# Performance work log

Hardware: AMD Instinct MI355X
Metric: run time of the kernel (lower is better)

The kernel has to match this reference:

```python
import jax, jax.numpy as jnp
import numpy as np

B, T, C, H = 2, 2048, 1024, 16
N = C // H
TM_DIM, TD_DIM = 32, 64
EPS = 1e-5 * 8 ** 2  # GroupNorm eps from the module


def setup_inputs() -> dict:
    key = jax.random.key(0)
    ks = jax.random.split(key, 16)
    nrm = lambda k, shp, s: jax.random.normal(k, shp, dtype=jnp.float32) * s
    uni = lambda k, shp, a: jax.random.uniform(k, shp, jnp.float32, -a, a)
    ddd = (jnp.arange(C, dtype=jnp.float32) / C).reshape(1, 1, C)
    return {
        "x": nrm(ks[0], (B, T, C), 1.0),
        "time_maa_x": 1.0 - ddd ** 0.5,
        "time_maa_w": 1.0 - ddd ** 0.5,
        "time_maa_k": 1.0 - ddd ** 0.5,
        "time_maa_v": 1.0 - (ddd ** 0.5 + 0.15),
        "time_maa_r": 1.0 - ddd ** 0.25,
        "time_maa_g": 1.0 - ddd ** 0.25,
        "time_maa_w1": uni(ks[1], (C, 5 * TM_DIM), 1e-4),
        "time_maa_w2": uni(ks[2], (5, TM_DIM, C), 1e-4),
        "time_decay": jnp.linspace(-6.0, -1.0, C).astype(jnp.float32).reshape(1, 1, C),
        "time_decay_w1": uni(ks[3], (C, TD_DIM), 1e-4),
        "time_decay_w2": uni(ks[4], (TD_DIM, C), 1e-4),
        "time_faaaa": nrm(ks[5], (H, N), 0.1),
        "W_r": nrm(ks[6], (C, C), C ** -0.5),
        "W_k": nrm(ks[7], (C, C), C ** -0.5),
        "W_v": nrm(ks[8], (C, C), C ** -0.5),
        "W_g": nrm(ks[9], (C, C), C ** -0.5),
        "W_o": nrm(ks[10], (C, C), C ** -0.5),
        "ln_w": jnp.ones((C,), jnp.float32),
        "ln_b": jnp.zeros((C,), jnp.float32),
    }


def _forward(x, tmx, tmw, tmk, tmv, tmr, tmg, maa_w1, maa_w2, tdecay, td_w1,
             td_w2, u, Wr, Wk, Wv, Wg, Wo, ln_w, ln_b):
    Bq, Tq, Cq = x.shape
    # time_shift: x[t-1] with zero at t=0
    xx = jnp.concatenate([jnp.zeros_like(x[:, :1]), x[:, :-1]], axis=1) - x
    xxx = x + xx * tmx
    t5 = jnp.tanh(xxx @ maa_w1).reshape(Bq, Tq, 5, TM_DIM)
    m = jnp.einsum('btfe,fec->fbtc', t5, maa_w2)  # [5,B,T,C] data-dependent mix
    xw = x + xx * (tmw + m[0])
    xk = x + xx * (tmk + m[1])
    xv = x + xx * (tmv + m[2])
    xr = x + xx * (tmr + m[3])
    xg = x + xx * (tmg + m[4])
    r = xr @ Wr
    k = xk @ Wk
    v = xv @ Wv
    g = jax.nn.silu(xg @ Wg)
    w = tdecay + jnp.tanh(xw @ td_w1) @ td_w2          # [B,T,C] log-log decay
    decay = jnp.exp(-jnp.exp(w))                        # in (0,1)
    to_tbhn = lambda a: a.reshape(Bq, Tq, H, N).transpose(1, 0, 2, 3)
    rT, kT, vT, dT = (to_tbhn(a) for a in (r, k, v, decay))

    def step(S, inp):  # S: [B,H,N,N] (key_dim i, value_dim j)
        r_t, k_t, v_t, d_t = inp
        kv = k_t[..., :, None] * v_t[..., None, :]
        y = jnp.einsum('bhi,bhij->bhj', r_t, S + u[None, :, :, None] * kv)
        return d_t[..., None] * S + kv, y

    S0 = jnp.zeros((Bq, H, N, N), x.dtype)
    _, ys = jax.lax.scan(step, S0, (rT, kT, vT, dT))
    y = ys.transpose(1, 0, 2, 3).reshape(Bq, Tq, Cq)
    # GroupNorm with H groups over channels
    yh = y.reshape(Bq, Tq, H, N)
    mu = yh.mean(-1, keepdims=True)
    var = yh.var(-1, keepdims=True)
    yn = (yh - mu) / jnp.sqrt(var + EPS)
    yn = (yn * ln_w.reshape(H, N) + ln_b.reshape(H, N)).reshape(Bq, Tq, Cq)
    return (yn * g) @ Wo


def reference(x, time_maa_x, time_maa_w, time_maa_k, time_maa_v, time_maa_r,
              time_maa_g, time_maa_w1, time_maa_w2, time_decay, time_decay_w1,
              time_decay_w2, time_faaaa, W_r, W_k, W_v, W_g, W_o, ln_w, ln_b):
    return _forward(x, time_maa_x, time_maa_w, time_maa_k, time_maa_v,
                    time_maa_r, time_maa_g, time_maa_w1, time_maa_w2,
                    time_decay, time_decay_w1, time_decay_w2, time_faaaa,
                    W_r, W_k, W_v, W_g, W_o, ln_w, ln_b)
```

## Files before the change

### kernel.cpp

```cpp
#include <hip/hip_runtime.h>
#include <hip/hip_bf16.h>
#include <cstdint>
#include <cstddef>

#define B_ 2
#define T_ 2048
#define C_ 1024
#define H_ 16
#define NCH 32
#define CHL 64

typedef unsigned short ushort_t;
typedef __bf16 bf16x8 __attribute__((ext_vector_type(8)));
typedef float f32x4 __attribute__((ext_vector_type(4)));

__device__ __forceinline__ ushort_t f2bf(float f) {
  union { float f; uint32_t u; } x; x.f = f;
  uint32_t r = x.u + 0x7fffu + ((x.u >> 16) & 1u);
  return (ushort_t)(r >> 16);
}
__device__ __forceinline__ float bf2f(ushort_t h) {
  union { uint32_t u; float f; } x; x.u = (uint32_t)h << 16; return x.f;
}

__device__ __forceinline__ void gload16(const void* g, void* l) {
  __builtin_amdgcn_global_load_lds(
      (const __attribute__((address_space(1))) void*)g,
      (__attribute__((address_space(3))) void*)l, 16, 0, 0);
}

#define FENCE() asm volatile("" ::: "memory")
#define BAR() do { FENCE(); __builtin_amdgcn_s_barrier(); FENCE(); } while (0)

__device__ __forceinline__ void stb(ushort_t* tile, int row, int col, ushort_t v) {
  *(ushort_t*)((char*)tile + row * 128 + ((col * 2) ^ ((row & 7) << 4))) = v;
}
__device__ __forceinline__ bf16x8 ldb(const ushort_t* tile, int row, int kbyte) {
  return *(const bf16x8*)((const char*)tile + row * 128 + (kbyte ^ ((row & 7) << 4)));
}

struct TDesc { const float* src; ushort_t* dst; int R, Cc, Cpad; };
struct TArgs { TDesc d[9]; };

__global__ __launch_bounds__(256) void init_kernel(
    TArgs args, const float* __restrict__ x, const float* __restrict__ tmx,
    ushort_t* __restrict__ xh, ushort_t* __restrict__ xxh,
    ushort_t* __restrict__ xxx) {
  if (blockIdx.z < 9) {
    TDesc D = args.d[blockIdx.z];
    int c0 = blockIdx.x * 32, r0 = blockIdx.y * 32;
    if (c0 >= D.Cpad || r0 >= D.R) return;
    __shared__ float tile[32][33];
    int tx = threadIdx.x & 31, ty = threadIdx.x >> 5;
#pragma unroll
    for (int i = 0; i < 32; i += 8) {
      int r = r0 + ty + i, c = c0 + tx;
      tile[ty + i][tx] = (r < D.R && c < D.Cc) ? D.src[(size_t)r * D.Cc + c] : 0.f;
    }
    __syncthreads();
#pragma unroll
    for (int i = 0; i < 32; i += 8) {
      int c = c0 + ty + i, r = r0 + tx;
      if (c < D.Cpad && r < D.R) D.dst[(size_t)c * D.R + r] = f2bf(tile[tx][ty + i]);
    }
    return;
  }
  int lin = (blockIdx.y * 32 + blockIdx.x) * 256 + threadIdx.x;
#pragma unroll
  for (int rep = 0; rep < 4; ++rep) {
    size_t idx = ((size_t)(rep * 262144 + lin)) * 4;
    int tt = (int)((idx >> 10) & (T_ - 1));
    int c = (int)(idx & (C_ - 1));
    float4 xv = *(const float4*)&x[idx];
    float4 xp;
    if (tt == 0) { xp.x = xp.y = xp.z = xp.w = 0.f; }
    else xp = *(const float4*)&x[idx - C_];
    float4 tm = *(const float4*)&tmx[c];
    float4 d;
    d.x = xp.x - xv.x; d.y = xp.y - xv.y; d.z = xp.z - xv.z; d.w = xp.w - xv.w;
    ushort4 a, b, cc;
    a.x = f2bf(xv.x); a.y = f2bf(xv.y); a.z = f2bf(xv.z); a.w = f2bf(xv.w);
    b.x = f2bf(d.x);  b.y = f2bf(d.y);  b.z = f2bf(d.z);  b.w = f2bf(d.w);
    cc.x = f2bf(xv.x + d.x * tm.x); cc.y = f2bf(xv.y + d.y * tm.y);
    cc.z = f2bf(xv.z + d.z * tm.z); cc.w = f2bf(xv.w + d.w * tm.w);
    *(ushort4*)&xh[idx] = a;
    *(ushort4*)&xxh[idx] = b;
    *(ushort4*)&xxx[idx] = cc;
  }
}

__global__ __launch_bounds__(256) void gemm_bt(
    const ushort_t* __restrict__ A, int lda,
    const ushort_t* __restrict__ Bt, int ldb,
    float* __restrict__ Cp, int ldc, int K) {
  __shared__ ushort_t sA[128 * 32];
  __shared__ ushort_t sB[128 * 32];
  const int t = threadIdx.x;
  const int l = t & 63;
  const int w = t >> 6;
  const int wm = w >> 1, wn = w & 1;
  const int m0 = blockIdx.x * 128, n0 = blockIdx.y * 128;
  const int lr = l & 15;
  const int lk = (l >> 4) * 8;

  f32x4 acc[4][4] = {};

  for (int kt = 0; kt < K; kt += 32) {
    __syncthreads();
#pragma unroll
    for (int it = 0; it < 2; ++it) {
      int cbase = it * 256 + w * 64;
      int ca = cbase + l;
      int row = ca >> 2, kc = ca & 3;
      gload16(A + (size_t)(m0 + row) * lda + kt + kc * 8, (char*)sA + (size_t)cbase * 16);
      gload16(Bt + (size_t)(n0 + row) * ldb + kt + kc * 8, (char*)sB + (size_t)cbase * 16);
    }
    __syncthreads();
    bf16x8 af[4], bfr[4];
#pragma unroll
    for (int mi = 0; mi < 4; ++mi)
      af[mi] = *(const bf16x8*)&sA[(wm * 64 + mi * 16 + lr) * 32 + lk];
#pragma unroll
    for (int ni = 0; ni < 4; ++ni)
      bfr[ni] = *(const bf16x8*)&sB[(wn * 64 + ni * 16 + lr) * 32 + lk];
#pragma unroll
    for (int mi = 0; mi < 4; ++mi)
#pragma unroll
      for (int ni = 0; ni < 4; ++ni)
        acc[mi][ni] = __builtin_amdgcn_mfma_f32_16x16x32_bf16(af[mi], bfr[ni], acc[mi][ni], 0, 0, 0);
  }
#pragma unroll
  for (int mi = 0; mi < 4; ++mi) {
#pragma unroll
    for (int ni = 0; ni < 4; ++ni) {
      int col = n0 + wn * 64 + ni * 16 + lr;
#pragma unroll
      for (int r = 0; r < 4; ++r) {
        int row = m0 + wm * 64 + mi * 16 + (l >> 4) * 4 + r;
        Cp[(size_t)row * ldc + col] = acc[mi][ni][r];
      }
    }
  }
}

__global__ __launch_bounds__(256) void gemm_bt32(
    const ushort_t* __restrict__ A, int lda,
    const ushort_t* __restrict__ Bt, int ldb,
    ushort_t* __restrict__ Cp, int ldc, int K) {
  __shared__ ushort_t sA[32 * 32];
  __shared__ ushort_t sB[128 * 32];
  const int t = threadIdx.x;
  const int l = t & 63;
  const int w = t >> 6;
  const int m0 = blockIdx.x * 32, n0 = blockIdx.y * 128;
  const int lr = l & 15, lk = (l >> 4) * 8;

  f32x4 acc[2][2] = {};
  for (int kt = 0; kt < K; kt += 32) {
    __syncthreads();
    if (t < 128) {
      int row = t >> 2, kc = t & 3;
      gload16(A + (size_t)(m0 + row) * lda + kt + kc * 8, (char*)sA + t * 16);
    }
#pragma unroll
    for (int it = 0; it < 2; ++it) {
      int ca = it * 256 + t;
      int row = ca >> 2, kc = ca & 3;
      gload16(Bt + (size_t)(n0 + row) * ldb + kt + kc * 8,
              (char*)sB + it * 4096 + w * 1024);
    }
    __syncthreads();
    bf16x8 af[2], bfr[2];
#pragma unroll
    for (int mi = 0; mi < 2; ++mi)
      af[mi] = *(const bf16x8*)&sA[(mi * 16 + lr) * 32 + lk];
#pragma unroll
    for (int ni = 0; ni < 2; ++ni)
      bfr[ni] = *(const bf16x8*)&sB[(w * 32 + ni * 16 + lr) * 32 + lk];
#pragma unroll
    for (int mi = 0; mi < 2; ++mi)
#pragma unroll
      for (int ni = 0; ni < 2; ++ni)
        acc[mi][ni] = __builtin_amdgcn_mfma_f32_16x16x32_bf16(af[mi], bfr[ni], acc[mi][ni], 0, 0, 0);
  }
#pragma unroll
  for (int mi = 0; mi < 2; ++mi)
#pragma unroll
    for (int ni = 0; ni < 2; ++ni) {
      int col = n0 + w * 32 + ni * 16 + lr;
#pragma unroll
      for (int r = 0; r < 4; ++r) {
        int row = m0 + mi * 16 + (l >> 4) * 4 + r;
        Cp[(size_t)row * ldc + col] = f2bf(tanhf(acc[mi][ni][r]));
      }
    }
}

struct PDesc { const ushort_t* A; const ushort_t* Bt; void* C; int epi; };
struct PArgs { PDesc d[4]; };

__global__ __launch_bounds__(512, 1) void gemm_proj256(PArgs args) {
  PDesc D = args.d[blockIdx.z];
  __shared__ ushort_t sMem[2][2][4][4096];
  const int tid = threadIdx.x;
  const int w = tid >> 6, l = tid & 63;
  const int wm = w >> 2, wn = w & 3;
  const int lr = l & 15, hi4 = l >> 4;
  const int m0 = blockIdx.x * 256, n0 = blockIdx.y * 256;

  const int srow = tid >> 3;
  const int scol = (((tid & 7) ^ (srow & 7)) << 3);
  const ushort_t* Abase = D.A + (size_t)(m0 + srow) * C_ + scol;
  const ushort_t* Bbase = D.Bt + (size_t)(n0 + srow) * C_ + scol;
  const int dst16 = tid * 16;

  f32x4 acc[8][4] = {};
  bf16x8 bfr[2][4];

#define STG_A(db, unit, kt) \
  gload16(Abase + (size_t)(unit) * 64 * C_ + (kt), (char*)&sMem[db][0][unit][0] + dst16)
#define STG_B(db, unit, kt) \
  gload16(Bbase + (size_t)(unit) * 64 * C_ + (kt), (char*)&sMem[db][1][unit][0] + dst16)

#define LDA_(b, p, i, kk)                                                      \
  (*(const bf16x8*)((const char*)&sMem[b][0][wm * 2 + ((p) >> 1)][0] +         \
                    (((2 * (p) + (i)) & 3) * 16 + lr) * 128 +                  \
                    ((((kk)*4 + hi4) ^ (lr & 7)) << 4)))
#define LDB_(b, ni, kk)                                                        \
  (*(const bf16x8*)((const char*)&sMem[b][1][wn][0] +                          \
                    ((ni)*16 + lr) * 128 + ((((kk)*4 + hi4) ^ (lr & 7)) << 4)))

#define PH(b, p, STAGES, VM)                                                   \
  do {                                                                         \
    bf16x8 a00, a10, a01, a11;                                                 \
    if ((p) == 0) {                                                            \
      _Pragma("unroll") for (int kk = 0; kk < 2; ++kk)                         \
      _Pragma("unroll") for (int ni = 0; ni < 4; ++ni)                         \
        bfr[kk][ni] = LDB_(b, ni, kk);                                         \
    }                                                                          \
    a00 = LDA_(b, p, 0, 0); a10 = LDA_(b, p, 1, 0);                            \
    a01 = LDA_(b, p, 0, 1); a11 = LDA_(b, p, 1, 1);                            \
    STAGES;                                                                    \
    VM;                                                                        \
    BAR();                                                                     \
    asm volatile("s_waitcnt lgkmcnt(0)" ::: "memory");                         \
    __builtin_amdgcn_sched_barrier(0);                                         \
    __builtin_amdgcn_s_setprio(1);                                             \
    _Pragma("unroll") for (int ni = 0; ni < 4; ++ni) {                         \
      acc[2 * (p)][ni] = __builtin_amdgcn_mfma_f32_16x16x32_bf16(              \
          a00, bfr[0][ni], acc[2 * (p)][ni], 0, 0, 0);                         \
      acc[2 * (p) + 1][ni] = __builtin_amdgcn_mfma_f32_16x16x32_bf16(          \
          a10, bfr[0][ni], acc[2 * (p) + 1][ni], 0, 0, 0);                     \
      acc[2 * (p)][ni] = __builtin_amdgcn_mfma_f32_16x16x32_bf16(              \
          a01, bfr[1][ni], acc[2 * (p)][ni], 0, 0, 0);                         \
      acc[2 * (p) + 1][ni] = __builtin_amdgcn_mfma_f32_16x16x32_bf16(          \
          a11, bfr[1][ni], acc[2 * (p) + 1][ni], 0, 0, 0);                     \
    }                                                                          \
    __builtin_amdgcn_s_setprio(0);                                             \
    BAR();                                                                     \
  } while (0)

#define TILE(b, kt1, kt2)                                                      \
  do {                                                                         \
    PH(b, 0, { STG_A((b) ^ 1, 1, kt1); STG_A((b) ^ 1, 3, kt1); }, );           \
    PH(b, 1, { STG_B(b, 0, kt2); STG_B(b, 1, kt2); },                          \
       asm volatile("s_waitcnt vmcnt(10)" ::: "memory"));                      \
    PH(b, 2, { STG_B(b, 2, kt2); STG_B(b, 3, kt2); }, );                       \
    PH(b, 3, { STG_A(b, 0, kt2); STG_A(b, 2, kt2); },                          \
       asm volatile("s_waitcnt vmcnt(8)" ::: "memory"));                       \
  } while (0)

  STG_B(0, 0, 0);  STG_B(0, 1, 0);
  STG_B(0, 2, 0);  STG_B(0, 3, 0);
  STG_A(0, 0, 0);  STG_A(0, 2, 0);
  STG_A(0, 1, 0);  STG_A(0, 3, 0);
  STG_B(1, 0, 64); STG_B(1, 1, 64);
  STG_B(1, 2, 64); STG_B(1, 3, 64);
  STG_A(1, 0, 64); STG_A(1, 2, 64);
  asm volatile("s_waitcnt vmcnt(8)" ::: "memory");
  BAR();

#pragma unroll 1
  for (int j = 0; j < 16; j += 2) {
    int ka1 = ((j + 1) & 15) * 64, ka2 = ((j + 2) & 15) * 64;
    int kb1 = ((j + 2) & 15) * 64, kb2 = ((j + 3) & 15) * 64;
    TILE(0, ka1, ka2);
    TILE(1, kb1, kb2);
  }
  asm volatile("s_waitcnt vmcnt(0)" ::: "memory");

  const int epi = D.epi;
#pragma unroll
  for (int mi = 0; mi < 8; ++mi)
#pragma unroll
    for (int ni = 0; ni < 4; ++ni) {
      int col = n0 + wn * 64 + ni * 16 + lr;
#pragma unroll
      for (int r = 0; r < 4; ++r) {
        int row = m0 + wm * 128 + mi * 16 + hi4 * 4 + r;
        float v = acc[mi][ni][r];
        size_t idx = (size_t)row * C_ + col;
        if (epi == 2) {
          v = v / (1.f + __expf(-v));
          ((ushort_t*)D.C)[idx] = f2bf(v);
        } else if (epi == 3) {
          ((ushort_t*)D.C)[idx] = f2bf(v);
        } else {
          ((float*)D.C)[idx] = v;
        }
      }
    }
#undef TILE
#undef PH
#undef LDB_
#undef LDA_
#undef STG_B
#undef STG_A
}

struct MixArgs { const float* tm[5]; ushort_t* dst[5]; };

__global__ __launch_bounds__(256) void fused_mix(
    const ushort_t* __restrict__ xh, const ushort_t* __restrict__ xxh,
    const ushort_t* __restrict__ t5, const ushort_t* __restrict__ w2t,
    MixArgs margs) {
  __shared__ ushort_t xs[64 * 128];
  __shared__ ushort_t xxs[64 * 128];
  __shared__ ushort_t sA[64 * 32];
  __shared__ ushort_t sB[128 * 32];
  const int t = threadIdx.x;
  const int l = t & 63;
  const int w = t >> 6;
  const int wm = w >> 1, wn = w & 1;
  const int m0 = blockIdx.x * 64, n0 = blockIdx.y * 128;
  const int lr = l & 15;
  const int lk = (l >> 4) * 8;

#pragma unroll
  for (int it = 0; it < 4; ++it) {
    int row = it * 16 + (t >> 4);
    int c8 = t & 15;
    gload16(xh + (size_t)(m0 + row) * C_ + n0 + c8 * 8, (char*)xs + row * 256 + c8 * 16);
    gload16(xxh + (size_t)(m0 + row) * C_ + n0 + c8 * 8, (char*)xxs + row * 256 + c8 * 16);
  }

  for (int f = 0; f < 5; ++f) {
    __syncthreads();
    {
      int row = t >> 2, c8 = t & 3;
      gload16(t5 + (size_t)(m0 + row) * 256 + f * 32 + c8 * 8, (char*)sA + t * 16);
    }
#pragma unroll
    for (int it = 0; it < 2; ++it) {
      int row = it * 64 + (t >> 2), c8 = t & 3;
      gload16(w2t + (size_t)(n0 + row) * 160 + f * 32 + c8 * 8,
              (char*)sB + it * 4096 + t * 16);
    }
    __syncthreads();
    bf16x8 af[2], bfr[4];
#pragma unroll
    for (int mi = 0; mi < 2; ++mi)
      af[mi] = *(const bf16x8*)&sA[(wm * 32 + mi * 16 + lr) * 32 + lk];
#pragma unroll
    for (int ni = 0; ni < 4; ++ni)
      bfr[ni] = *(const bf16x8*)&sB[(wn * 64 + ni * 16 + lr) * 32 + lk];
    f32x4 acc[2][4] = {};
#pragma unroll
    for (int mi = 0; mi < 2; ++mi)
#pragma unroll
      for (int ni = 0; ni < 4; ++ni)
        acc[mi][ni] = __builtin_amdgcn_mfma_f32_16x16x32_bf16(af[mi], bfr[ni], acc[mi][ni], 0, 0, 0);
    const float* tmf = margs.tm[f];
    ushort_t* dst = margs.dst[f];
#pragma unroll
    for (int mi = 0; mi < 2; ++mi) {
#pragma unroll
      for (int ni = 0; ni < 4; ++ni) {
        int cl = wn * 64 + ni * 16 + lr;
        int col = n0 + cl;
        float tmv = tmf[col];
#pragma unroll
        for (int r = 0; r < 4; ++r) {
          int rl = wm * 32 + mi * 16 + (l >> 4) * 4 + r;
          int row = m0 + rl;
          float xv = bf2f(xs[rl * 128 + cl]);
          float xxv = bf2f(xxs[rl * 128 + cl]);
          dst[(size_t)row * C_ + col] = f2bf(xv + xxv * (tmv + acc[mi][ni][r]));
        }
      }
    }
  }
}

__global__ __launch_bounds__(256) void chunk_local(
    const ushort_t* __restrict__ rxh, const ushort_t* __restrict__ kxh,
    const float* __restrict__ vx, const ushort_t* __restrict__ t5d,
    const ushort_t* __restrict__ w2t, const float* __restrict__ tdec,
    const float* __restrict__ u, float* __restrict__ Mt,
    float* __restrict__ aLg, ushort_t* __restrict__ rAg,
    ushort_t* __restrict__ yo) {
  int c = blockIdx.x, bh = blockIdx.y;
  int b = bh >> 4, h = bh & 15;
  __shared__ ushort_t sRA[64 * 64], sKA[64 * 64], sKh[64 * 64], sKl[64 * 64],
                      sVh[64 * 64], sVl[64 * 64], sP[64 * 64];
  __shared__ float sLam[64 * 64];
  __shared__ float qsum[4][64];
  __shared__ float ruk[64];
  const int tid = threadIdx.x;
  const int i = tid & 63;
  const int q = tid >> 6;
  size_t base = ((size_t)b * T_ + (size_t)c * CHL) * C_ + h * 64;
  size_t cb = ((size_t)c * 32 + bh);
  const int trow0 = b * T_ + c * CHL;

  const int lr0 = tid & 15, hi0 = (tid & 63) >> 4;

#pragma unroll
  for (int p = 0; p < 2; ++p) {
    int L = p * 256 + tid;
    int r = L >> 3, u8 = L & 7;
    int sc = (u8 ^ (r & 7)) * 8;
    gload16(t5d + (size_t)(trow0 + r) * 128 + sc, (char*)sRA + L * 16);
    gload16(w2t + (size_t)(h * 64 + r) * 64 + sc, (char*)sKA + L * 16);
  }
  asm volatile("s_waitcnt vmcnt(0)" ::: "memory");
  __syncthreads();
  {
    f32x4 accL[4] = {};
#pragma unroll
    for (int kk = 0; kk < 2; ++kk) {
      bf16x8 bw = ldb(sKA, q * 16 + lr0, kk * 64 + hi0 * 16);
#pragma unroll
      for (int mi = 0; mi < 4; ++mi) {
        bf16x8 at = ldb(sRA, mi * 16 + lr0, kk * 64 + hi0 * 16);
        accL[mi] = __builtin_amdgcn_mfma_f32_16x16x32_bf16(at, bw, accL[mi], 0, 0, 0);
      }
    }
    float tdv = tdec[h * 64 + q * 16 + lr0];
#pragma unroll
    for (int mi = 0; mi < 4; ++mi)
#pragma unroll
      for (int rr = 0; rr < 4; ++rr)
        sLam[(mi * 16 + hi0 * 4 + rr) * 64 + q * 16 + lr0] = __expf(tdv + accL[mi][rr]);
  }
  __syncthreads();

  float lam[16];
  float run = 0.f;
#pragma unroll
  for (int s = 0; s < 16; ++s) {
    lam[s] = sLam[(q * 16 + s) * 64 + i];
    run += lam[s];
  }
  qsum[q][i] = run;
  __syncthreads();
  float pre = 0.f, ct = 0.f;
#pragma unroll
  for (int qq = 0; qq < 4; ++qq) {
    float vq = qsum[qq][i];
    ct += vq;
    if (qq < q) pre += vq;
  }
  float uu = u[h * 64 + i];
  float ci = pre;
#pragma unroll
  for (int s = 0; s < 16; ++s) {
    int t = q * 16 + s;
    ci += lam[s];
    float cl = ci - lam[s];
    size_t o = base + (size_t)t * C_ + i;
    float rv = bf2f(rxh[o]), kv = bf2f(kxh[o]), vv = vx[o];
    ushort_t ra = f2bf(rv * __expf(-cl));
    stb(sRA, t, i, ra);
    rAg[cb * 4096 + t * 64 + i] = ra;
    stb(sKA, t, i, f2bf(kv * __expf(ci)));
    float kal = kv * __expf(ci - ct);
    ushort_t khv = f2bf(kal);
    stb(sKh, i, t, khv);
    stb(sKl, i, t, f2bf(kal - bf2f(khv)));
    ushort_t vhv = f2bf(vv);
    stb(sVh, i, t, vhv);
    stb(sVl, i, t, f2bf(vv - bf2f(vhv)));
    float rr = rv * uu * kv;
#pragma unroll
    for (int m = 32; m; m >>= 1) rr += __shfl_xor(rr, m);
    if (i == 0) ruk[t] = rr;
  }
  if (q == 0) aLg[cb * 64 + i] = __expf(-ct);
  __syncthreads();

  const int l = tid & 63, w = tid >> 6;
  const int wm = w >> 1, wn = w & 1;
  const int lr = l & 15, hi4 = l >> 4;

  {
    f32x4 accP[2][2] = {};
#pragma unroll
    for (int kk = 0; kk < 2; ++kk) {
      bf16x8 af[2], bf_[2];
#pragma unroll
      for (int mi = 0; mi < 2; ++mi) af[mi] = ldb(sRA, wm * 32 + mi * 16 + lr, kk * 64 + hi4 * 16);
#pragma unroll
      for (int ni = 0; ni < 2; ++ni) bf_[ni] = ldb(sKA, wn * 32 + ni * 16 + lr, kk * 64 + hi4 * 16);
#pragma unroll
      for (int mi = 0; mi < 2; ++mi)
#pragma unroll
        for (int ni = 0; ni < 2; ++ni)
          accP[mi][ni] = __builtin_amdgcn_mfma_f32_16x16x32_bf16(af[mi], bf_[ni], accP[mi][ni], 0, 0, 0);
    }
#pragma unroll
    for (int mi = 0; mi < 2; ++mi)
#pragma unroll
      for (int ni = 0; ni < 2; ++ni)
#pragma unroll
        for (int r = 0; r < 4; ++r) {
          int tl = wm * 32 + mi * 16 + hi4 * 4 + r, sl = wn * 32 + ni * 16 + lr;
          float v = accP[mi][ni][r];
          v = sl < tl ? v : (sl == tl ? ruk[tl] : 0.f);
          stb(sP, tl, sl, f2bf(v));
        }
  }
  __syncthreads();

  f32x4 accY[2][2] = {}, accM[2][2] = {};
#pragma unroll
  for (int kk = 0; kk < 2; ++kk) {
    bf16x8 pa[2], vhA[2], vlA[2], vhB[2], vlB[2], khB[2], klB[2];
#pragma unroll
    for (int mi = 0; mi < 2; ++mi) {
      int rw = wm * 32 + mi * 16 + lr;
      pa[mi] = ldb(sP, rw, kk * 64 + hi4 * 16);
      vhA[mi] = ldb(sVh, rw, kk * 64 + hi4 * 16);
      vlA[mi] = ldb(sVl, rw, kk * 64 + hi4 * 16);
    }
#pragma unroll
    for (int ni = 0; ni < 2; ++ni) {
      int rw = wn * 32 + ni * 16 + lr;
      vhB[ni] = ldb(sVh, rw, kk * 64 + hi4 * 16);
      vlB[ni] = ldb(sVl, rw, kk * 64 + hi4 * 16);
      khB[ni] = ldb(sKh, rw, kk * 64 + hi4 * 16);
      klB[ni] = ldb(sKl, rw, kk * 64 + hi4 * 16);
    }
#pragma unroll
    for (int mi = 0; mi < 2; ++mi)
#pragma unroll
      for (int ni = 0; ni < 2; ++ni) {
        accY[mi][ni] = __builtin_amdgcn_mfma_f32_16x16x32_bf16(pa[mi], vhB[ni], accY[mi][ni], 0, 0, 0);
        accY[mi][ni] = __builtin_amdgcn_mfma_f32_16x16x32_bf16(pa[mi], vlB[ni], accY[mi][ni], 0, 0, 0);
        accM[mi][ni] = __builtin_amdgcn_mfma_f32_16x16x32_bf16(vhA[mi], khB[ni], accM[mi][ni], 0, 0, 0);
        accM[mi][ni] = __builtin_amdgcn_mfma_f32_16x16x32_bf16(vhA[mi], klB[ni], accM[mi][ni], 0, 0, 0);
        accM[mi][ni] = __builtin_amdgcn_mfma_f32_16x16x32_bf16(vlA[mi], khB[ni], accM[mi][ni], 0, 0, 0);
      }
  }
#pragma unroll
  for (int mi = 0; mi < 2; ++mi)
#pragma unroll
    for (int ni = 0; ni < 2; ++ni)
#pragma unroll
      for (int r = 0; r < 4; ++r) {
        int rw = wm * 32 + mi * 16 + hi4 * 4 + r;
        int cw = wn * 32 + ni * 16 + lr;
        yo[base + (size_t)rw * C_ + cw] = f2bf(accY[mi][ni][r]);
        Mt[cb * 4096 + rw * 64 + cw] = accM[mi][ni][r];
      }
}

__global__ __launch_bounds__(128) void combine2(
    const float* __restrict__ Mt, const float* __restrict__ aLg,
    ushort_t* __restrict__ S0h, ushort_t* __restrict__ S0l) {
  int bh = blockIdx.x >> 3;
  int ij = ((blockIdx.x & 7) * 128 + threadIdx.x) * 4;
  int i = ij & 63;
  const float* Mp = Mt + (size_t)bh * 4096 + ij;
  const float* Pp = aLg + (size_t)bh * 64 + i;
  ushort_t* Hp = S0h + (size_t)bh * 4096 + ij;
  ushort_t* Lp = S0l + (size_t)bh * 4096 + ij;
  float4 s = {0.f, 0.f, 0.f, 0.f};
  float4 m = *(const float4*)Mp;
  float4 p = *(const float4*)Pp;
  for (int c = 0; c < NCH; ++c) {
    float4 mn, pn;
    if (c < NCH - 1) {
      mn = *(const float4*)(Mp + (size_t)(c + 1) * (32 * 4096));
      pn = *(const float4*)(Pp + (size_t)(c + 1) * (32 * 64));
    }
    size_t o = (size_t)c * (32 * 4096);
    ushort4 hi, lo;
    hi.x = f2bf(s.x); lo.x = f2bf(s.x - bf2f(hi.x));
    hi.y = f2bf(s.y); lo.y = f2bf(s.y - bf2f(hi.y));
    hi.z = f2bf(s.z); lo.z = f2bf(s.z - bf2f(hi.z));
    hi.w = f2bf(s.w); lo.w = f2bf(s.w - bf2f(hi.w));
    *(ushort4*)(Hp + o) = hi;
    *(ushort4*)(Lp + o) = lo;
    s.x = p.x * s.x + m.x; s.y = p.y * s.y + m.y;
    s.z = p.z * s.z + m.z; s.w = p.w * s.w + m.w;
    m = mn; p = pn;
  }
}

__global__ __launch_bounds__(256) void inter_gn(
    const ushort_t* __restrict__ rAg, const ushort_t* __restrict__ S0h,
    const ushort_t* __restrict__ S0l, const ushort_t* __restrict__ yin,
    const ushort_t* __restrict__ gx, const float* __restrict__ lnw,
    const float* __restrict__ lnb, ushort_t* __restrict__ Z) {
  int c = blockIdx.x, bh = blockIdx.y;
  int b = bh >> 4, h = bh & 15;
  __shared__ ushort_t sRA[64 * 64], sSh[64 * 64], sSl[64 * 64];
  __shared__ float st[64][2][2];
  const int tid = threadIdx.x;
  size_t cb = ((size_t)c * 32 + bh) * 4096;
#pragma unroll
  for (int it = 0; it < 2; ++it) {
    int lb = tid * 32 + it * 16;
    int row = lb >> 7, wi = lb & 127;
    int so = row * 128 + (wi ^ ((row & 7) << 4));
    *(uint4*)((char*)sRA + so) = *(const uint4*)((const char*)(rAg + cb) + lb);
    *(uint4*)((char*)sSh + so) = *(const uint4*)((const char*)(S0h + cb) + lb);
    *(uint4*)((char*)sSl + so) = *(const uint4*)((const char*)(S0l + cb) + lb);
  }
  const int l = tid & 63, w = tid >> 6;
  const int wm = w >> 1, wn = w & 1;
  const int lr = l & 15, hi4 = l >> 4;
  size_t base = ((size_t)b * T_ + (size_t)c * CHL) * C_ + h * 64;

  f32x4 acc[2][2];
#pragma unroll
  for (int mi = 0; mi < 2; ++mi)
#pragma unroll
    for (int ni = 0; ni < 2; ++ni)
#pragma unroll
      for (int r = 0; r < 4; ++r)
        acc[mi][ni][r] = bf2f(yin[base + (size_t)(wm * 32 + mi * 16 + hi4 * 4 + r) * C_ +
                                  wn * 32 + ni * 16 + lr]);
  __syncthreads();
#pragma unroll
  for (int kk = 0; kk < 2; ++kk) {
    bf16x8 af[2], bh_[2], bl_[2];
#pragma unroll
    for (int mi = 0; mi < 2; ++mi) af[mi] = ldb(sRA, wm * 32 + mi * 16 + lr, kk * 64 + hi4 * 16);
#pragma unroll
    for (int ni = 0; ni < 2; ++ni) {
      bh_[ni] = ldb(sSh, wn * 32 + ni * 16 + lr, kk * 64 + hi4 * 16);
      bl_[ni] = ldb(sSl, wn * 32 + ni * 16 + lr, kk * 64 + hi4 * 16);
    }
#pragma unroll
    for (int mi = 0; mi < 2; ++mi)
#pragma unroll
      for (int ni = 0; ni < 2; ++ni) {
        acc[mi][ni] = __builtin_amdgcn_mfma_f32_16x16x32_bf16(af[mi], bh_[ni], acc[mi][ni], 0, 0, 0);
        acc[mi][ni] = __builtin_amdgcn_mfma_f32_16x16x32_bf16(af[mi], bl_[ni], acc[mi][ni], 0, 0, 0);
      }
  }
#pragma unroll
  for (int mi = 0; mi < 2; ++mi)
#pragma unroll
    for (int r = 0; r < 4; ++r) {
      int row = wm * 32 + mi * 16 + hi4 * 4 + r;
      float s1 = acc[mi][0][r] + acc[mi][1][r];
      float s2 = acc[mi][0][r] * acc[mi][0][r] + acc[mi][1][r] * acc[mi][1][r];
#pragma unroll
      for (int m = 1; m < 16; m <<= 1) { s1 += __shfl_xor(s1, m); s2 += __shfl_xor(s2, m); }
      if (lr == 0) { st[row][wn][0] = s1; st[row][wn][1] = s2; }
    }
  __syncthreads();
#pragma unroll
  for (int mi = 0; mi < 2; ++mi)
#pragma unroll
    for (int ni = 0; ni < 2; ++ni)
#pragma unroll
      for (int r = 0; r < 4; ++r) {
        int row = wm * 32 + mi * 16 + hi4 * 4 + r;
        int jl = wn * 32 + ni * 16 + lr;
        float S1 = st[row][0][0] + st[row][1][0];
        float S2 = st[row][0][1] + st[row][1][1];
        float mu = S1 * (1.f / 64.f);
        float var = S2 * (1.f / 64.f) - mu * mu;
        float rs = rsqrtf(var + 6.4e-4f);
        int col = h * 64 + jl;
        size_t o = base + (size_t)row * C_ + jl;
        float yn = (acc[mi][ni][r] - mu) * rs * lnw[col] + lnb[col];
        Z[o] = f2bf(yn * bf2f(gx[o]));
      }
}

extern "C" void kernel_launch(void* const* d_in, const int* in_sizes, int n_in,
                              void* d_out, int out_size, void* d_ws, size_t ws_size,
                              hipStream_t stream) {
  const float* x    = (const float*)d_in[0];
  const float* tmx  = (const float*)d_in[1];
  const float* tmw  = (const float*)d_in[2];
  const float* tmk  = (const float*)d_in[3];
  const float* tmv  = (const float*)d_in[4];
  const float* tmr  = (const float*)d_in[5];
  const float* tmg  = (const float*)d_in[6];
  const float* maaw1 = (const float*)d_in[7];
  const float* maaw2 = (const float*)d_in[8];
  const float* tdec = (const float*)d_in[9];
  const float* tdw1 = (const float*)d_in[10];
  const float* tdw2 = (const float*)d_in[11];
  const float* u    = (const float*)d_in[12];
  const float* Wr   = (const float*)d_in[13];
  const float* Wk   = (const float*)d_in[14];
  const float* Wv   = (const float*)d_in[15];
  const float* Wg   = (const float*)d_in[16];
  const float* Wo   = (const float*)d_in[17];
  const float* lnw  = (const float*)d_in[18];
  const float* lnb  = (const float*)d_in[19];

  char* ws = (char*)d_ws;
  const size_t MB = 1ull << 20;
  ushort_t* xh     = (ushort_t*)(ws + 0);
  ushort_t* xxh    = (ushort_t*)(ws + 8 * MB);
  ushort_t* xxx    = (ushort_t*)(ws + 16 * MB);
  ushort_t* WrT    = (ushort_t*)(ws + 24 * MB);
  ushort_t* WkT    = (ushort_t*)(ws + 26 * MB);
  ushort_t* WvT    = (ushort_t*)(ws + 28 * MB);
  ushort_t* WgT    = (ushort_t*)(ws + 30 * MB);
  ushort_t* WoT    = (ushort_t*)(ws + 32 * MB);
  ushort_t* maaW1T = (ushort_t*)(ws + 34 * MB);
  ushort_t* tdW1T  = (ushort_t*)(ws + 35 * MB);
  ushort_t* tdW2T  = (ushort_t*)(ws + 35 * MB + 256 * 1024);
  ushort_t* maaW2T = (ushort_t*)(ws + 35 * MB + 512 * 1024);
  ushort_t* t5     = (ushort_t*)(ws + 36 * MB);
  ushort_t* t5d    = (ushort_t*)(ws + 38 * MB);
  ushort_t* Xm[5];
  for (int f = 0; f < 5; ++f) Xm[f] = (ushort_t*)(ws + 40 * MB + (size_t)f * 8 * MB);
  float*    Mtb = (float*)(ws + 40 * MB);
  ushort_t* S0h = (ushort_t*)(ws + 56 * MB);
  ushort_t* S0l = (ushort_t*)(ws + 64 * MB);
  ushort_t* rAg = (ushort_t*)(ws + 72 * MB);
  ushort_t* rbh = (ushort_t*)(ws + 80 * MB);
  ushort_t* kbh = (ushort_t*)(ws + 96 * MB);
  float* vb   = (float*)(ws + 112 * MB);
  ushort_t* gbh = (ushort_t*)(ws + 128 * MB);
  float* aLg  = (float*)(ws + 144 * MB);
  ushort_t* yb = (ushort_t*)(ws + 0);
  ushort_t* Zb = (ushort_t*)(ws + 16 * MB);

  TArgs ta;
  ta.d[0] = TDesc{Wr,    WrT,    1024, 1024, 1024};
  ta.d[1] = TDesc{Wk,    WkT,    1024, 1024, 1024};
  ta.d[2] = TDesc{Wv,    WvT,    1024, 1024, 1024};
  ta.d[3] = TDesc{Wg,    WgT,    1024, 1024, 1024};
  ta.d[4] = TDesc{Wo,    WoT,    1024, 1024, 1024};
  ta.d[5] = TDesc{maaw1, maaW1T, 1024, 160,  256};
  ta.d[6] = TDesc{tdw1,  tdW1T,  1024, 64,   128};
  ta.d[7] = TDesc{tdw2,  tdW2T,  64,   1024, 1024};
  ta.d[8] = TDesc{maaw2, maaW2T, 160,  1024, 1024};
  init_kernel<<<dim3(32, 32, 10), 256, 0, stream>>>(ta, x, tmx, xh, xxh, xxx);

  gemm_bt32<<<dim3(128, 2), 256, 0, stream>>>(xxx, C_, maaW1T, C_, t5, 256, C_);

  MixArgs ma;
  ma.tm[0] = tmw; ma.tm[1] = tmk; ma.tm[2] = tmv; ma.tm[3] = tmr; ma.tm[4] = tmg;
  for (int f = 0; f < 5; ++f) ma.dst[f] = Xm[f];
  fused_mix<<<dim3(64, 8), 256, 0, stream>>>(xh, xxh, t5, maaW2T, ma);

  PArgs pa;
  pa.d[0] = PDesc{Xm[3], WrT, rbh, 3};
  pa.d[1] = PDesc{Xm[1], WkT, kbh, 3};
  pa.d[2] = PDesc{Xm[2], WvT, vb, 0};
  pa.d[3] = PDesc{Xm[4], WgT, gbh, 2};
  gemm_proj256<<<dim3(16, 4, 4), 512, 0, stream>>>(pa);

  gemm_bt32<<<dim3(128, 1), 256, 0, stream>>>(Xm[0], C_, tdW1T, C_, t5d, 128, C_);

  chunk_local<<<dim3(NCH, B_ * H_), 256, 0, stream>>>(rbh, kbh, vb, t5d, tdW2T, tdec,
                                                      u, Mtb, aLg, rAg, yb);
  combine2<<<256, 128, 0, stream>>>(Mtb, aLg, S0h, S0l);
  inter_gn<<<dim3(NCH, B_ * H_), 256, 0, stream>>>(rAg, S0h, S0l, yb, gbh, lnw, lnb, Zb);

  gemm_bt<<<dim3(32, 8), 256, 0, stream>>>(Zb, C_, WoT, C_, (float*)d_out, C_, C_);
}
```

Measured before the change: 199.5 us.

## Retile projection GEMM to 256x128 tiles with K=32 double buffer and 2 blocks/CU

Rewrites the four-way projection GEMM so each block computes a 256x128 tile with 32-wide K steps and a simple double-buffered LDS pipeline, replacing the 256x256, K=64 phased schedule. LDS use drops and launch bounds allow two blocks per CU, and the grid doubles to 512 blocks. The goal is better occupancy and CU coverage on the 256-CU part, which had only 256 blocks. The cost is less reuse per tile, more barriers per K, and a new swizzle scheme that could cause bank conflicts.

After: 202.8 us. Within noise of the previous version (+1.7%).

```diff
diff --git a/kernel.cpp b/kernel.cpp
--- a/kernel.cpp
+++ b/kernel.cpp
@@ -199,93 +199,71 @@
 struct PDesc { const ushort_t* A; const ushort_t* Bt; void* C; int epi; };
 struct PArgs { PDesc d[4]; };
 
-__global__ __launch_bounds__(512, 1) void gemm_proj256(PArgs args) {
+__global__ __launch_bounds__(512, 2) void gemm_proj256(PArgs args) {
   PDesc D = args.d[blockIdx.z];
-  __shared__ ushort_t sMem[2][2][4][4096];
+  __shared__ ushort_t sMem[2][3][4096];
   const int tid = threadIdx.x;
   const int w = tid >> 6, l = tid & 63;
   const int wm = w >> 2, wn = w & 3;
   const int lr = l & 15, hi4 = l >> 4;
-  const int m0 = blockIdx.x * 256, n0 = blockIdx.y * 256;
-
-  const int srow = tid >> 3;
-  const int scol = (((tid & 7) ^ (srow & 7)) << 3);
-  const ushort_t* Abase = D.A + (size_t)(m0 + srow) * C_ + scol;
-  const ushort_t* Bbase = D.Bt + (size_t)(n0 + srow) * C_ + scol;
+  const int m0 = blockIdx.x * 256, n0 = blockIdx.y * 128;
+
+  const int srow = tid >> 2;
+  const int schunk = (((tid & 3) ^ ((tid >> 3) & 3))) * 8;
+  const ushort_t* Ab0 = D.A + (size_t)(m0 + srow) * C_ + schunk;
+  const ushort_t* Ab1 = Ab0 + (size_t)128 * C_;
+  const ushort_t* Bb  = D.Bt + (size_t)(n0 + srow) * C_ + schunk;
   const int dst16 = tid * 16;
-
-  f32x4 acc[8][4] = {};
-  bf16x8 bfr[2][4];
-
-#define STG_A(db, unit, kt) \
-  gload16(Abase + (size_t)(unit) * 64 * C_ + (kt), (char*)&sMem[db][0][unit][0] + dst16)
-#define STG_B(db, unit, kt) \
-  gload16(Bbase + (size_t)(unit) * 64 * C_ + (kt), (char*)&sMem[db][1][unit][0] + dst16)
-
-#define LDA_(b, p, i, kk)                                                      \
-  (*(const bf16x8*)((const char*)&sMem[b][0][wm * 2 + ((p) >> 1)][0] +         \
-                    (((2 * (p) + (i)) & 3) * 16 + lr) * 128 +                  \
-                    ((((kk)*4 + hi4) ^ (lr & 7)) << 4)))
-#define LDB_(b, ni, kk)                                                        \
-  (*(const bf16x8*)((const char*)&sMem[b][1][wn][0] +                          \
-                    ((ni)*16 + lr) * 128 + ((((kk)*4 + hi4) ^ (lr & 7)) << 4)))
-
-#define PH(b, p, STAGES, VM)                                                   \
-  do {                                                                         \
-    bf16x8 a00, a10, a01, a11;                                                 \
-    if ((p) == 0) {                                                            \
-      _Pragma("unroll") for (int kk = 0; kk < 2; ++kk)                         \
-      _Pragma("unroll") for (int ni = 0; ni < 4; ++ni)                         \
-        bfr[kk][ni] = LDB_(b, ni, kk);                                         \
-    }                                                                          \
-    a00 = LDA_(b, p, 0, 0); a10 = LDA_(b, p, 1, 0);                            \
-    a01 = LDA_(b, p, 0, 1); a11 = LDA_(b, p, 1, 1);                            \
-    STAGES;                                                                    \
-    VM;                                                                        \
-    BAR();                                                                     \
-    asm volatile("s_waitcnt lgkmcnt(0)" ::: "memory");                         \
-    __builtin_amdgcn_sched_barrier(0);                                         \
-    __builtin_amdgcn_s_setprio(1);                                             \
-    _Pragma("unroll") for (int ni = 0; ni < 4; ++ni) {                         \
-      acc[2 * (p)][ni] = __builtin_amdgcn_mfma_f32_16x16x32_bf16(              \
-          a00, bfr[0][ni], acc[2 * (p)][ni], 0, 0, 0);                         \
-      acc[2 * (p) + 1][ni] = __builtin_amdgcn_mfma_f32_16x16x32_bf16(          \
-          a10, bfr[0][ni], acc[2 * (p) + 1][ni], 0, 0, 0);                     \
-      acc[2 * (p)][ni] = __builtin_amdgcn_mfma_f32_16x16x32_bf16(              \
-          a01, bfr[1][ni], acc[2 * (p)][ni], 0, 0, 0);                         \
-      acc[2 * (p) + 1][ni] = __builtin_amdgcn_mfma_f32_16x16x32_bf16(          \
-          a11, bfr[1][ni], acc[2 * (p) + 1][ni], 0, 0, 0);                     \
-    }                                                                          \
-    __builtin_amdgcn_s_setprio(0);                                             \
-    BAR();                                                                     \
+  const int slotA = (hi4 ^ ((lr >> 1) & 3)) << 4;
+
+  f32x4 acc[8][2] = {};
+
+#define STG(b, kt)                                              \
+  do {                                                          \
+    gload16(Ab0 + (kt), (char*)&sMem[b][0][0] + dst16);         \
+    gload16(Ab1 + (kt), (char*)&sMem[b][1][0] + dst16);         \
+    gload16(Bb  + (kt), (char*)&sMem[b][2][0] + dst16);         \
   } while (0)
 
-#define TILE(b, kt1, kt2)                                                      \
-  do {                                                                         \
-    PH(b, 0, { STG_A((b) ^ 1, 1, kt1); STG_A((b) ^ 1, 3, kt1); }, );           \
-    PH(b, 1, { STG_B(b, 0, kt2); STG_B(b, 1, kt2); },                          \
-       asm volatile("s_waitcnt vmcnt(10)" ::: "memory"));                      \
-    PH(b, 2, { STG_B(b, 2, kt2); STG_B(b, 3, kt2); }, );                       \
-    PH(b, 3, { STG_A(b, 0, kt2); STG_A(b, 2, kt2); },                          \
-       asm volatile("s_waitcnt vmcnt(8)" ::: "memory"));                       \
+#define LDA(b, mi) \
+  (*(const bf16x8*)((const char*)&sMem[b][wm][0] + ((mi)*16 + lr) * 64 + slotA))
+#define LDB(b, ni) \
+  (*(const bf16x8*)((const char*)&sMem[b][2][0] + (wn * 32 + (ni)*16 + lr) * 64 + slotA))
+
+#define COMP(b)                                                               \
+  do {                                                                        \
+    bf16x8 b0 = LDB(b, 0), b1 = LDB(b, 1);                                    \
+    __builtin_amdgcn_s_setprio(1);                                            \
+    _Pragma("unroll") for (int mi = 0; mi < 8; ++mi) {                        \
+      bf16x8 af = LDA(b, mi);                                                 \
+      acc[mi][0] = __builtin_amdgcn_mfma_f32_16x16x32_bf16(af, b0, acc[mi][0], 0, 0, 0); \
+      acc[mi][1] = __builtin_amdgcn_mfma_f32_16x16x32_bf16(af, b1, acc[mi][1], 0, 0, 0); \
+    }                                                                         \
+    __builtin_amdgcn_s_setprio(0);                                            \
   } while (0)
 
-  STG_B(0, 0, 0);  STG_B(0, 1, 0);
-  STG_B(0, 2, 0);  STG_B(0, 3, 0);
-  STG_A(0, 0, 0);  STG_A(0, 2, 0);
-  STG_A(0, 1, 0);  STG_A(0, 3, 0);
-  STG_B(1, 0, 64); STG_B(1, 1, 64);
-  STG_B(1, 2, 64); STG_B(1, 3, 64);
-  STG_A(1, 0, 64); STG_A(1, 2, 64);
-  asm volatile("s_waitcnt vmcnt(8)" ::: "memory");
+#define BODY(b, jj)                                                           \
+  do {                                                                        \
+    COMP(b);                                                                  \
+    BAR();                                                                    \
+    if ((jj) < 30) {                                                          \
+      STG(b, ((jj) + 2) * 32);                                                \
+      asm volatile("s_waitcnt vmcnt(3)" ::: "memory");                        \
+    } else if ((jj) == 30) {                                                  \
+      asm volatile("s_waitcnt vmcnt(0)" ::: "memory");                        \
+    }                                                                         \
+    BAR();                                                                    \
+  } while (0)
+
+  STG(0, 0);
+  STG(1, 32);
+  asm volatile("s_waitcnt vmcnt(3)" ::: "memory");
   BAR();
 
 #pragma unroll 1
-  for (int j = 0; j < 16; j += 2) {
-    int ka1 = ((j + 1) & 15) * 64, ka2 = ((j + 2) & 15) * 64;
-    int kb1 = ((j + 2) & 15) * 64, kb2 = ((j + 3) & 15) * 64;
-    TILE(0, ka1, ka2);
-    TILE(1, kb1, kb2);
+  for (int j = 0; j < 32; j += 2) {
+    BODY(0, j);
+    BODY(1, j + 1);
   }
   asm volatile("s_waitcnt vmcnt(0)" ::: "memory");
 
@@ -293,8 +271,8 @@
 #pragma unroll
   for (int mi = 0; mi < 8; ++mi)
 #pragma unroll
-    for (int ni = 0; ni < 4; ++ni) {
-      int col = n0 + wn * 64 + ni * 16 + lr;
+    for (int ni = 0; ni < 2; ++ni) {
+      int col = n0 + wn * 32 + ni * 16 + lr;
 #pragma unroll
       for (int r = 0; r < 4; ++r) {
         int row = m0 + wm * 128 + mi * 16 + hi4 * 4 + r;
@@ -310,12 +288,11 @@
         }
       }
     }
-#undef TILE
-#undef PH
-#undef LDB_
-#undef LDA_
-#undef STG_B
-#undef STG_A
+#undef BODY
+#undef COMP
+#undef LDB
+#undef LDA
+#undef STG
 }
 
 struct MixArgs { const float* tm[5]; ushort_t* dst[5]; };
@@ -761,7 +738,7 @@
   pa.d[1] = PDesc{Xm[1], WkT, kbh, 3};
   pa.d[2] = PDesc{Xm[2], WvT, vb, 0};
   pa.d[3] = PDesc{Xm[4], WgT, gbh, 2};
-  gemm_proj256<<<dim3(16, 4, 4), 512, 0, stream>>>(pa);
+  gemm_proj256<<<dim3(16, 8, 4), 512, 0, stream>>>(pa);
 
   gemm_bt32<<<dim3(128, 1), 256, 0, stream>>>(Xm[0], C_, tdW1T, C_, t5d, 128, C_);
 
```
